# Kernel optimization log

Measured on AMD Instinct MI355X. Metric: run time of the kernel, lower is better.

The kernel has to match this reference:

```python
import jax, jax.numpy as jnp
import numpy as np

NUM_SRC1, NUM_DST1 = 2_000_000, 131_072
NUM_SRC2, NUM_DST2 = 131_072, 8_192
E1, E2 = NUM_DST1 * 15, NUM_DST2 * 15
F_IN, F_H = 128, 128


def setup_inputs() -> dict:
    key = jax.random.key(0)
    ks = jax.random.split(key, 10)
    return {
        "x": jax.random.normal(ks[0], (NUM_SRC1, F_IN), dtype=jnp.float32),
        "edge1_src": jax.random.randint(ks[1], (E1,), 0, NUM_SRC1, dtype=jnp.int32),
        "edge1_dst": jax.random.randint(ks[2], (E1,), 0, NUM_DST1, dtype=jnp.int32),
        "edge2_src": jax.random.randint(ks[3], (E2,), 0, NUM_SRC2, dtype=jnp.int32),
        "edge2_dst": jax.random.randint(ks[4], (E2,), 0, NUM_DST2, dtype=jnp.int32),
        "num_dst1": NUM_DST1,
        "num_dst2": NUM_DST2,
        "W_self1": jax.random.normal(ks[5], (F_IN, F_H), dtype=jnp.float32) * 0.05,
        "W_neigh1": jax.random.normal(ks[6], (F_IN, F_H), dtype=jnp.float32) * 0.05,
        "b1": jnp.zeros((F_H,), dtype=jnp.float32),
        "W_self2": jax.random.normal(ks[7], (F_H, F_H), dtype=jnp.float32) * 0.05,
        "W_neigh2": jax.random.normal(ks[8], (F_H, F_H), dtype=jnp.float32) * 0.05,
        "b2": jnp.zeros((F_H,), dtype=jnp.float32),
    }


def _sage_mean(h_src, h_dst, e_src, e_dst, num_dst, W_self, W_neigh, b):
    # mean-aggregate neighbor feats per dst, then linear transforms (DGL SAGEConv, aggr='mean')
    agg = jax.ops.segment_sum(h_src[e_src], e_dst, num_segments=num_dst)  # [num_dst, F]
    deg = jax.ops.segment_sum(jnp.ones((e_dst.shape[0],), h_src.dtype), e_dst,
                              num_segments=num_dst)
    mean = agg / jnp.maximum(deg, 1.0)[:, None]
    return h_dst @ W_self + mean @ W_neigh + b


def reference(x, edge1_src, edge1_dst, edge2_src, edge2_dst, num_dst1, num_dst2,
              W_self1, W_neigh1, b1, W_self2, W_neigh2, b2):
    h_dst = x[:num_dst1]
    h = _sage_mean(x, h_dst, edge1_src, edge1_dst, num_dst1, W_self1, W_neigh1, b1)
    h = jax.nn.relu(h)
    h_dst2 = h[:num_dst2]
    out = _sage_mean(h, h_dst2, edge2_src, edge2_dst, num_dst2, W_self2, W_neigh2, b2)
    return out
```

## Files before the change

### kernel.cpp

```cpp
#include <hip/hip_runtime.h>

static constexpr int FDIM = 128;
static constexpr int ND1  = 131072;
static constexpr int ND2  = 8192;
static constexpr int PADW = 64;
static constexpr int LDP  = 56;
static constexpr int AML  = 136;

using bf16x8 = __attribute__((ext_vector_type(8))) short;
using u16x8  = __attribute__((ext_vector_type(8))) unsigned short;
using f32x4  = __attribute__((ext_vector_type(4))) float;

static __device__ __forceinline__ unsigned short f2bf(float f) {
  unsigned u = __float_as_uint(f);
  u = (u + 0x7FFFu + ((u >> 16) & 1u)) >> 16;
  return (unsigned short)u;
}
static __device__ __forceinline__ float bf2f(unsigned short s) {
  return __uint_as_float(((unsigned)s) << 16);
}

__global__ void build_pad(const int* __restrict__ e1s, const int* __restrict__ e1d,
                          const int* __restrict__ e2s, const int* __restrict__ e2d,
                          int* __restrict__ cnt1, int* __restrict__ cnt2,
                          int* __restrict__ pad1, int* __restrict__ pad2,
                          int E1, int E2, int nb_fill,
                          const float* __restrict__ Ws1, const float* __restrict__ Wn1,
                          unsigned short* __restrict__ Wt1,
                          const float* __restrict__ Ws2, const float* __restrict__ Wn2,
                          unsigned short* __restrict__ Wt2) {
  if ((int)blockIdx.x >= nb_fill) {
    int t = (blockIdx.x - nb_fill) * 256 + threadIdx.x;
    int which = t >> 15;
    int r = t & 32767;
    int col = r >> 8, k = r & 255;
    const float* Ws = which ? Ws2 : Ws1;
    const float* Wn = which ? Wn2 : Wn1;
    unsigned short* Wt = which ? Wt2 : Wt1;
    float v = (k < 128) ? Ws[k * 128 + col] : Wn[(k - 128) * 128 + col];
    Wt[col * 256 + k] = f2bf(v);
    return;
  }
  const int n1 = E1 >> 2, n2 = E2 >> 2;
  int t = blockIdx.x * 256 + threadIdx.x;
  if (t < n1) {
    int4 d = ((const int4*)e1d)[t];
    int4 s = ((const int4*)e1s)[t];
    int p;
    p = atomicAdd(&cnt1[d.x], 1); if (p < PADW) pad1[d.x * PADW + p] = s.x;
    p = atomicAdd(&cnt1[d.y], 1); if (p < PADW) pad1[d.y * PADW + p] = s.y;
    p = atomicAdd(&cnt1[d.z], 1); if (p < PADW) pad1[d.z * PADW + p] = s.z;
    p = atomicAdd(&cnt1[d.w], 1); if (p < PADW) pad1[d.w * PADW + p] = s.w;
  } else if (t < n1 + n2) {
    int4 d = ((const int4*)e2d)[t - n1];
    int4 s = ((const int4*)e2s)[t - n1];
    int p;
    p = atomicAdd(&cnt2[d.x], 1); if (p < PADW) pad2[d.x * PADW + p] = s.x;
    p = atomicAdd(&cnt2[d.y], 1); if (p < PADW) pad2[d.y * PADW + p] = s.y;
    p = atomicAdd(&cnt2[d.z], 1); if (p < PADW) pad2[d.z * PADW + p] = s.z;
    p = atomicAdd(&cnt2[d.w], 1); if (p < PADW) pad2[d.w * PADW + p] = s.w;
  }
  if (blockIdx.x == 0) {
    int tt = threadIdx.x;
    if (tt < (E1 & 3)) {
      int e = E1 - 1 - tt, d = e1d[e];
      int p = atomicAdd(&cnt1[d], 1); if (p < PADW) pad1[d * PADW + p] = e1s[e];
    }
    int t2 = tt - 8;
    if (t2 >= 0 && t2 < (E2 & 3)) {
      int e = E2 - 1 - t2, d = e2d[e];
      int p = atomicAdd(&cnt2[d], 1); if (p < PADW) pad2[d * PADW + p] = e2s[e];
    }
  }
}

template<bool L1>
__global__ __launch_bounds__(256)
void fused_layer(const void* __restrict__ selfp,
                 const int* __restrict__ pad, const int* __restrict__ cnt,
                 const unsigned short* __restrict__ Wt,
                 const float* __restrict__ bias,
                 void* __restrict__ Outp)
{
  __shared__ unsigned short AmL[128 * AML];
  __shared__ unsigned short Asb[128 * LDP];
  __shared__ unsigned short Wsb[128 * LDP];
  const int tid  = threadIdx.x;
  const int lane = tid & 63;
  const int w    = tid >> 6;
  const int half = lane >> 5;
  const int sub  = lane & 31;
  const int row0 = blockIdx.x * 128;

  for (int i = 0; i < 16; ++i) {
    const int rl   = w * 32 + i * 2 + half;
    const int row  = row0 + rl;
    const int degt = cnt[row];
    const int deg  = degt < PADW ? degt : PADW;
    float ax = 0.f, ay = 0.f, az = 0.f, aw = 0.f;
    for (int base = 0; base < deg; base += 32) {
      int t = base + sub;
      int idx = pad[(size_t)row * PADW + (t < deg ? t : deg - 1)];
      const int lim = (deg - base) < 32 ? (deg - base) : 32;
      for (int b = 0; b < lim; b += 8) {
        if (L1) {
          float4 v[8];
          #pragma unroll
          for (int j = 0; j < 8; ++j) {
            int e = __shfl(idx, half * 32 + b + j);
            v[j] = *(const float4*)((const float*)selfp + (size_t)e * FDIM + sub * 4);
          }
          #pragma unroll
          for (int j = 0; j < 8; ++j) {
            float mk = (b + j) < lim ? 1.f : 0.f;
            ax = fmaf(v[j].x, mk, ax); ay = fmaf(v[j].y, mk, ay);
            az = fmaf(v[j].z, mk, az); aw = fmaf(v[j].w, mk, aw);
          }
        } else {
          ushort4 v[8];
          #pragma unroll
          for (int j = 0; j < 8; ++j) {
            int e = __shfl(idx, half * 32 + b + j);
            v[j] = *(const ushort4*)((const unsigned short*)selfp + (size_t)e * FDIM + sub * 4);
          }
          #pragma unroll
          for (int j = 0; j < 8; ++j) {
            float mk = (b + j) < lim ? 1.f : 0.f;
            ax = fmaf(bf2f(v[j].x), mk, ax); ay = fmaf(bf2f(v[j].y), mk, ay);
            az = fmaf(bf2f(v[j].z), mk, az); aw = fmaf(bf2f(v[j].w), mk, aw);
          }
        }
      }
    }
    const float inv = 1.f / (float)(degt > 1 ? degt : 1);
    ushort4 o;
    o.x = f2bf(ax * inv); o.y = f2bf(ay * inv);
    o.z = f2bf(az * inv); o.w = f2bf(aw * inv);
    *(ushort4*)&AmL[rl * AML + sub * 4] = o;
  }
  __syncthreads();

  const int p = lane & 15;
  const int q = lane >> 4;
  f32x4 acc[2][8];
  #pragma unroll
  for (int m = 0; m < 2; ++m)
    #pragma unroll
    for (int n = 0; n < 8; ++n) acc[m][n] = (f32x4){0.f, 0.f, 0.f, 0.f};

  const int sr = tid >> 1;
  const int sk = (tid & 1) * 16;

  for (int c = 0; c < 8; ++c) {
    const int kc = c * 32;
    const int kl = kc & 127;
    {
      const unsigned short* wsrc = Wt + (size_t)sr * 256 + kc + sk;
      u16x8 a = *(const u16x8*)(wsrc);
      u16x8 b = *(const u16x8*)(wsrc + 8);
      *(u16x8*)&Wsb[sr * LDP + sk]     = a;
      *(u16x8*)&Wsb[sr * LDP + sk + 8] = b;
    }
    if (c >= 4) {
      u16x8 a = *(const u16x8*)&AmL[sr * AML + kl + sk];
      u16x8 b = *(const u16x8*)&AmL[sr * AML + kl + sk + 8];
      *(u16x8*)&Asb[sr * LDP + sk]     = a;
      *(u16x8*)&Asb[sr * LDP + sk + 8] = b;
    } else if (!L1) {
      const unsigned short* asrc =
          (const unsigned short*)selfp + (size_t)(row0 + sr) * FDIM + kl + sk;
      u16x8 a = *(const u16x8*)(asrc);
      u16x8 b = *(const u16x8*)(asrc + 8);
      *(u16x8*)&Asb[sr * LDP + sk]     = a;
      *(u16x8*)&Asb[sr * LDP + sk + 8] = b;
    } else {
      const float* asrc = (const float*)selfp + (size_t)(row0 + sr) * FDIM + kl + sk;
      float4 f0 = *(const float4*)(asrc);
      float4 f1 = *(const float4*)(asrc + 4);
      float4 f2 = *(const float4*)(asrc + 8);
      float4 f3 = *(const float4*)(asrc + 12);
      u16x8 a, b;
      a[0] = f2bf(f0.x); a[1] = f2bf(f0.y); a[2] = f2bf(f0.z); a[3] = f2bf(f0.w);
      a[4] = f2bf(f1.x); a[5] = f2bf(f1.y); a[6] = f2bf(f1.z); a[7] = f2bf(f1.w);
      b[0] = f2bf(f2.x); b[1] = f2bf(f2.y); b[2] = f2bf(f2.z); b[3] = f2bf(f2.w);
      b[4] = f2bf(f3.x); b[5] = f2bf(f3.y); b[6] = f2bf(f3.z); b[7] = f2bf(f3.w);
      *(u16x8*)&Asb[sr * LDP + sk]     = a;
      *(u16x8*)&Asb[sr * LDP + sk + 8] = b;
    }
    __syncthreads();
    bf16x8 af[2];
    #pragma unroll
    for (int m = 0; m < 2; ++m)
      af[m] = *(const bf16x8*)&Asb[(w * 32 + m * 16 + p) * LDP + q * 8];
    #pragma unroll
    for (int n = 0; n < 8; ++n) {
      bf16x8 bfr = *(const bf16x8*)&Wsb[(n * 16 + p) * LDP + q * 8];
      acc[0][n] = __builtin_amdgcn_mfma_f32_16x16x32_bf16(af[0], bfr, acc[0][n], 0, 0, 0);
      acc[1][n] = __builtin_amdgcn_mfma_f32_16x16x32_bf16(af[1], bfr, acc[1][n], 0, 0, 0);
    }
    __syncthreads();
  }

  #pragma unroll
  for (int n = 0; n < 8; ++n) {
    const int col = n * 16 + p;
    const float bv = bias[col];
    #pragma unroll
    for (int m = 0; m < 2; ++m) {
      #pragma unroll
      for (int r = 0; r < 4; ++r) {
        float y = acc[m][n][r] + bv;
        if (L1) y = fmaxf(y, 0.f);
        const size_t grow = (size_t)(row0 + w * 32 + m * 16 + q * 4 + r);
        if (L1) ((unsigned short*)Outp)[grow * FDIM + col] = f2bf(y);
        else    ((float*)Outp)[grow * FDIM + col] = y;
      }
    }
  }
}

extern "C" void kernel_launch(void* const* d_in, const int* in_sizes, int n_in,
                              void* d_out, int out_size, void* d_ws, size_t ws_size,
                              hipStream_t stream) {
  const float* x   = (const float*)d_in[0];
  const int*   e1s = (const int*)d_in[1];
  const int*   e1d = (const int*)d_in[2];
  const int*   e2s = (const int*)d_in[3];
  const int*   e2d = (const int*)d_in[4];
  const float* Ws1 = (const float*)d_in[7];
  const float* Wn1 = (const float*)d_in[8];
  const float* b1  = (const float*)d_in[9];
  const float* Ws2 = (const float*)d_in[10];
  const float* Wn2 = (const float*)d_in[11];
  const float* b2  = (const float*)d_in[12];
  const int E1 = in_sizes[1];
  const int E2 = in_sizes[3];

  char* pw = (char*)d_ws;
  unsigned short* h   = (unsigned short*)pw; pw += (size_t)ND1 * FDIM * 2;
  unsigned short* Wt1 = (unsigned short*)pw; pw += (size_t)FDIM * 256 * 2;
  unsigned short* Wt2 = (unsigned short*)pw; pw += (size_t)FDIM * 256 * 2;
  int* pad1 = (int*)pw; pw += (size_t)ND1 * PADW * 4;
  int* pad2 = (int*)pw; pw += (size_t)ND2 * PADW * 4;
  int* cnt1 = (int*)pw; pw += (size_t)ND1 * 4;
  int* cnt2 = (int*)pw; pw += (size_t)ND2 * 4;

  hipMemsetAsync(cnt1, 0, (size_t)(ND1 + ND2) * 4, stream);

  const int n4 = (E1 >> 2) + (E2 >> 2);
  const int nb_fill = (n4 + 255) / 256;
  build_pad<<<nb_fill + 256, 256, 0, stream>>>(e1s, e1d, e2s, e2d, cnt1, cnt2,
                                               pad1, pad2, E1, E2, nb_fill,
                                               Ws1, Wn1, Wt1, Ws2, Wn2, Wt2);

  fused_layer<true ><<<ND1 / 128, 256, 0, stream>>>(x, pad1, cnt1, Wt1, b1, h);
  fused_layer<false><<<ND2 / 128, 256, 0, stream>>>(h, pad2, cnt2, Wt2, b2, (float*)d_out);
}
```

Before: 442.1 us.

## Split layer-1 into separate gather-mean and MFMA GEMM kernels

Layer 1 is split from one fused gather-plus-GEMM kernel into a standalone gather/mean kernel that writes a bf16 aggregate to workspace, followed by a separate MFMA GEMM kernel. The gather kernel uses many small blocks (two rows per wave) to raise occupancy and memory-level parallelism for the random gathers, which the fused kernel's large LDS footprint limited. The layer-2 CSR build moves into that gather launch's tail blocks. The cost is an extra round trip of the aggregate through global memory (about 32 MB write plus read) and one more launch.

```diff
diff --git a/kernel.cpp b/kernel.cpp
--- a/kernel.cpp
+++ b/kernel.cpp
@@ -20,15 +20,13 @@
   return __uint_as_float(((unsigned)s) << 16);
 }
 
-__global__ void build_pad(const int* __restrict__ e1s, const int* __restrict__ e1d,
-                          const int* __restrict__ e2s, const int* __restrict__ e2d,
-                          int* __restrict__ cnt1, int* __restrict__ cnt2,
-                          int* __restrict__ pad1, int* __restrict__ pad2,
-                          int E1, int E2, int nb_fill,
-                          const float* __restrict__ Ws1, const float* __restrict__ Wn1,
-                          unsigned short* __restrict__ Wt1,
-                          const float* __restrict__ Ws2, const float* __restrict__ Wn2,
-                          unsigned short* __restrict__ Wt2) {
+__global__ void build1(const int* __restrict__ e1s, const int* __restrict__ e1d,
+                       int* __restrict__ cnt1, int* __restrict__ pad1,
+                       int E1, int nb_fill,
+                       const float* __restrict__ Ws1, const float* __restrict__ Wn1,
+                       unsigned short* __restrict__ Wt1,
+                       const float* __restrict__ Ws2, const float* __restrict__ Wn2,
+                       unsigned short* __restrict__ Wt2) {
   if ((int)blockIdx.x >= nb_fill) {
     int t = (blockIdx.x - nb_fill) * 256 + threadIdx.x;
     int which = t >> 15;
@@ -41,7 +39,7 @@
     Wt[col * 256 + k] = f2bf(v);
     return;
   }
-  const int n1 = E1 >> 2, n2 = E2 >> 2;
+  const int n1 = E1 >> 2;
   int t = blockIdx.x * 256 + threadIdx.x;
   if (t < n1) {
     int4 d = ((const int4*)e1d)[t];
@@ -51,14 +49,6 @@
     p = atomicAdd(&cnt1[d.y], 1); if (p < PADW) pad1[d.y * PADW + p] = s.y;
     p = atomicAdd(&cnt1[d.z], 1); if (p < PADW) pad1[d.z * PADW + p] = s.z;
     p = atomicAdd(&cnt1[d.w], 1); if (p < PADW) pad1[d.w * PADW + p] = s.w;
-  } else if (t < n1 + n2) {
-    int4 d = ((const int4*)e2d)[t - n1];
-    int4 s = ((const int4*)e2s)[t - n1];
-    int p;
-    p = atomicAdd(&cnt2[d.x], 1); if (p < PADW) pad2[d.x * PADW + p] = s.x;
-    p = atomicAdd(&cnt2[d.y], 1); if (p < PADW) pad2[d.y * PADW + p] = s.y;
-    p = atomicAdd(&cnt2[d.z], 1); if (p < PADW) pad2[d.z * PADW + p] = s.z;
-    p = atomicAdd(&cnt2[d.w], 1); if (p < PADW) pad2[d.w * PADW + p] = s.w;
   }
   if (blockIdx.x == 0) {
     int tt = threadIdx.x;
@@ -66,21 +56,161 @@
       int e = E1 - 1 - tt, d = e1d[e];
       int p = atomicAdd(&cnt1[d], 1); if (p < PADW) pad1[d * PADW + p] = e1s[e];
     }
-    int t2 = tt - 8;
-    if (t2 >= 0 && t2 < (E2 & 3)) {
-      int e = E2 - 1 - t2, d = e2d[e];
-      int p = atomicAdd(&cnt2[d], 1); if (p < PADW) pad2[d * PADW + p] = e2s[e];
-    }
-  }
-}
-
-template<bool L1>
+  }
+}
+
 __global__ __launch_bounds__(256)
-void fused_layer(const void* __restrict__ selfp,
-                 const int* __restrict__ pad, const int* __restrict__ cnt,
-                 const unsigned short* __restrict__ Wt,
-                 const float* __restrict__ bias,
-                 void* __restrict__ Outp)
+void gather_mean1(const float* __restrict__ src, const int* __restrict__ pad,
+                  const int* __restrict__ cnt, unsigned short* __restrict__ out,
+                  int nrows, int nb_gather,
+                  const int* __restrict__ e2s, const int* __restrict__ e2d,
+                  int* __restrict__ cnt2, int* __restrict__ pad2, int E2) {
+  if ((int)blockIdx.x >= nb_gather) {
+    const int n2 = E2 >> 2;
+    int t = (blockIdx.x - nb_gather) * 256 + threadIdx.x;
+    if (t < n2) {
+      int4 d = ((const int4*)e2d)[t];
+      int4 s = ((const int4*)e2s)[t];
+      int p;
+      p = atomicAdd(&cnt2[d.x], 1); if (p < PADW) pad2[d.x * PADW + p] = s.x;
+      p = atomicAdd(&cnt2[d.y], 1); if (p < PADW) pad2[d.y * PADW + p] = s.y;
+      p = atomicAdd(&cnt2[d.z], 1); if (p < PADW) pad2[d.z * PADW + p] = s.z;
+      p = atomicAdd(&cnt2[d.w], 1); if (p < PADW) pad2[d.w * PADW + p] = s.w;
+    }
+    if (blockIdx.x == (unsigned)nb_gather) {
+      int tt = threadIdx.x;
+      if (tt < (E2 & 3)) {
+        int e = E2 - 1 - tt, d = e2d[e];
+        int p = atomicAdd(&cnt2[d], 1); if (p < PADW) pad2[d * PADW + p] = e2s[e];
+      }
+    }
+    return;
+  }
+  const int lane = threadIdx.x & 63;
+  const int half = lane >> 5;
+  const int sub  = lane & 31;
+  const int wid  = (int)((blockIdx.x * 256u + threadIdx.x) >> 6);
+  const int row  = wid * 2 + half;
+  if (row >= nrows) return;
+  const int degt = cnt[row];
+  const int deg  = degt < PADW ? degt : PADW;
+  float ax = 0.f, ay = 0.f, az = 0.f, aw = 0.f;
+  for (int base = 0; base < deg; base += 32) {
+    int t = base + sub;
+    int idx = pad[(size_t)row * PADW + (t < deg ? t : deg - 1)];
+    const int lim = (deg - base) < 32 ? (deg - base) : 32;
+    for (int b = 0; b < lim; b += 8) {
+      float4 v[8];
+      #pragma unroll
+      for (int j = 0; j < 8; ++j) {
+        int e = __shfl(idx, half * 32 + b + j);
+        v[j] = *(const float4*)(src + (size_t)e * FDIM + sub * 4);
+      }
+      #pragma unroll
+      for (int j = 0; j < 8; ++j) {
+        float mk = (b + j) < lim ? 1.f : 0.f;
+        ax = fmaf(v[j].x, mk, ax); ay = fmaf(v[j].y, mk, ay);
+        az = fmaf(v[j].z, mk, az); aw = fmaf(v[j].w, mk, aw);
+      }
+    }
+  }
+  const float inv = 1.f / (float)(degt > 1 ? degt : 1);
+  ushort4 o;
+  o.x = f2bf(ax * inv); o.y = f2bf(ay * inv);
+  o.z = f2bf(az * inv); o.w = f2bf(aw * inv);
+  *(ushort4*)(out + (size_t)row * FDIM + sub * 4) = o;
+}
+
+__global__ __launch_bounds__(256)
+void gemm_mfma1(const float* __restrict__ Ax,
+                const unsigned short* __restrict__ Am,
+                const unsigned short* __restrict__ Wt,
+                const float* __restrict__ bias,
+                unsigned short* __restrict__ Out) {
+  __shared__ unsigned short Asb[128 * LDP];
+  __shared__ unsigned short Wsb[128 * LDP];
+  const int tid  = threadIdx.x;
+  const int lane = tid & 63;
+  const int w    = tid >> 6;
+  const int row0 = blockIdx.x * 128;
+  const int p    = lane & 15;
+  const int q    = lane >> 4;
+
+  f32x4 acc[2][8];
+  #pragma unroll
+  for (int m = 0; m < 2; ++m)
+    #pragma unroll
+    for (int n = 0; n < 8; ++n) acc[m][n] = (f32x4){0.f, 0.f, 0.f, 0.f};
+
+  const int sr = tid >> 1;
+  const int sk = (tid & 1) * 16;
+
+  for (int c = 0; c < 8; ++c) {
+    const int kc = c * 32;
+    const int kl = kc & 127;
+    {
+      const unsigned short* wsrc = Wt + (size_t)sr * 256 + kc + sk;
+      u16x8 a = *(const u16x8*)(wsrc);
+      u16x8 b = *(const u16x8*)(wsrc + 8);
+      *(u16x8*)&Wsb[sr * LDP + sk]     = a;
+      *(u16x8*)&Wsb[sr * LDP + sk + 8] = b;
+    }
+    if (c >= 4) {
+      const unsigned short* asrc = Am + (size_t)(row0 + sr) * FDIM + kl + sk;
+      u16x8 a = *(const u16x8*)(asrc);
+      u16x8 b = *(const u16x8*)(asrc + 8);
+      *(u16x8*)&Asb[sr * LDP + sk]     = a;
+      *(u16x8*)&Asb[sr * LDP + sk + 8] = b;
+    } else {
+      const float* asrc = Ax + (size_t)(row0 + sr) * FDIM + kl + sk;
+      float4 f0 = *(const float4*)(asrc);
+      float4 f1 = *(const float4*)(asrc + 4);
+      float4 f2 = *(const float4*)(asrc + 8);
+      float4 f3 = *(const float4*)(asrc + 12);
+      u16x8 a, b;
+      a[0] = f2bf(f0.x); a[1] = f2bf(f0.y); a[2] = f2bf(f0.z); a[3] = f2bf(f0.w);
+      a[4] = f2bf(f1.x); a[5] = f2bf(f1.y); a[6] = f2bf(f1.z); a[7] = f2bf(f1.w);
+      b[0] = f2bf(f2.x); b[1] = f2bf(f2.y); b[2] = f2bf(f2.z); b[3] = f2bf(f2.w);
+      b[4] = f2bf(f3.x); b[5] = f2bf(f3.y); b[6] = f2bf(f3.z); b[7] = f2bf(f3.w);
+      *(u16x8*)&Asb[sr * LDP + sk]     = a;
+      *(u16x8*)&Asb[sr * LDP + sk + 8] = b;
+    }
+    __syncthreads();
+    bf16x8 af[2];
+    #pragma unroll
+    for (int m = 0; m < 2; ++m)
+      af[m] = *(const bf16x8*)&Asb[(w * 32 + m * 16 + p) * LDP + q * 8];
+    #pragma unroll
+    for (int n = 0; n < 8; ++n) {
+      bf16x8 bfr = *(const bf16x8*)&Wsb[(n * 16 + p) * LDP + q * 8];
+      acc[0][n] = __builtin_amdgcn_mfma_f32_16x16x32_bf16(af[0], bfr, acc[0][n], 0, 0, 0);
+      acc[1][n] = __builtin_amdgcn_mfma_f32_16x16x32_bf16(af[1], bfr, acc[1][n], 0, 0, 0);
+    }
+    __syncthreads();
+  }
+
+  #pragma unroll
+  for (int n = 0; n < 8; ++n) {
+    const int col = n * 16 + p;
+    const float bv = bias[col];
+    #pragma unroll
+    for (int m = 0; m < 2; ++m) {
+      #pragma unroll
+      for (int r = 0; r < 4; ++r) {
+        float y = fmaxf(acc[m][n][r] + bv, 0.f);
+        const size_t grow = (size_t)(row0 + w * 32 + m * 16 + q * 4 + r);
+        Out[grow * FDIM + col] = f2bf(y);
+      }
+    }
+  }
+}
+
+__global__ __launch_bounds__(256)
+void fused_layer2(const unsigned short* __restrict__ selfp,
+                  const int* __restrict__ pad, const int* __restrict__ cnt,
+                  const unsigned short* __restrict__ Wt,
+                  const float* __restrict__ bias,
+                  float* __restrict__ Outp)
 {
   __shared__ unsigned short AmL[128 * AML];
   __shared__ unsigned short Asb[128 * LDP];
@@ -103,32 +233,17 @@
       int idx = pad[(size_t)row * PADW + (t < deg ? t : deg - 1)];
       const int lim = (deg - base) < 32 ? (deg - base) : 32;
       for (int b = 0; b < lim; b += 8) {
-        if (L1) {
-          float4 v[8];
-          #pragma unroll
-          for (int j = 0; j < 8; ++j) {
-            int e = __shfl(idx, half * 32 + b + j);
-            v[j] = *(const float4*)((const float*)selfp + (size_t)e * FDIM + sub * 4);
-          }
-          #pragma unroll
-          for (int j = 0; j < 8; ++j) {
-            float mk = (b + j) < lim ? 1.f : 0.f;
-            ax = fmaf(v[j].x, mk, ax); ay = fmaf(v[j].y, mk, ay);
-            az = fmaf(v[j].z, mk, az); aw = fmaf(v[j].w, mk, aw);
-          }
-        } else {
-          ushort4 v[8];
-          #pragma unroll
-          for (int j = 0; j < 8; ++j) {
-            int e = __shfl(idx, half * 32 + b + j);
-            v[j] = *(const ushort4*)((const unsigned short*)selfp + (size_t)e * FDIM + sub * 4);
-          }
-          #pragma unroll
-          for (int j = 0; j < 8; ++j) {
-            float mk = (b + j) < lim ? 1.f : 0.f;
-            ax = fmaf(bf2f(v[j].x), mk, ax); ay = fmaf(bf2f(v[j].y), mk, ay);
-            az = fmaf(bf2f(v[j].z), mk, az); aw = fmaf(bf2f(v[j].w), mk, aw);
-          }
+        ushort4 v[8];
+        #pragma unroll
+        for (int j = 0; j < 8; ++j) {
+          int e = __shfl(idx, half * 32 + b + j);
+          v[j] = *(const ushort4*)(selfp + (size_t)e * FDIM + sub * 4);
+        }
+        #pragma unroll
+        for (int j = 0; j < 8; ++j) {
+          float mk = (b + j) < lim ? 1.f : 0.f;
+          ax = fmaf(bf2f(v[j].x), mk, ax); ay = fmaf(bf2f(v[j].y), mk, ay);
+          az = fmaf(bf2f(v[j].z), mk, az); aw = fmaf(bf2f(v[j].w), mk, aw);
         }
       }
     }
@@ -166,26 +281,12 @@
       u16x8 b = *(const u16x8*)&AmL[sr * AML + kl + sk + 8];
       *(u16x8*)&Asb[sr * LDP + sk]     = a;
       *(u16x8*)&Asb[sr * LDP + sk + 8] = b;
-    } else if (!L1) {
-      const unsigned short* asrc =
-          (const unsigned short*)selfp + (size_t)(row0 + sr) * FDIM + kl + sk;
+    } else {
+      const unsigned short* asrc = selfp + (size_t)(row0 + sr) * FDIM + kl + sk;
       u16x8 a = *(const u16x8*)(asrc);
       u16x8 b = *(const u16x8*)(asrc + 8);
       *(u16x8*)&Asb[sr * LDP + sk]     = a;
       *(u16x8*)&Asb[sr * LDP + sk + 8] = b;
-    } else {
-      const float* asrc = (const float*)selfp + (size_t)(row0 + sr) * FDIM + kl + sk;
-      float4 f0 = *(const float4*)(asrc);
-      float4 f1 = *(const float4*)(asrc + 4);
-      float4 f2 = *(const float4*)(asrc + 8);
-      float4 f3 = *(const float4*)(asrc + 12);
-      u16x8 a, b;
-      a[0] = f2bf(f0.x); a[1] = f2bf(f0.y); a[2] = f2bf(f0.z); a[3] = f2bf(f0.w);
-      a[4] = f2bf(f1.x); a[5] = f2bf(f1.y); a[6] = f2bf(f1.z); a[7] = f2bf(f1.w);
-      b[0] = f2bf(f2.x); b[1] = f2bf(f2.y); b[2] = f2bf(f2.z); b[3] = f2bf(f2.w);
-      b[4] = f2bf(f3.x); b[5] = f2bf(f3.y); b[6] = f2bf(f3.z); b[7] = f2bf(f3.w);
-      *(u16x8*)&Asb[sr * LDP + sk]     = a;
-      *(u16x8*)&Asb[sr * LDP + sk + 8] = b;
     }
     __syncthreads();
     bf16x8 af[2];
@@ -210,10 +311,8 @@
       #pragma unroll
       for (int r = 0; r < 4; ++r) {
         float y = acc[m][n][r] + bv;
-        if (L1) y = fmaxf(y, 0.f);
         const size_t grow = (size_t)(row0 + w * 32 + m * 16 + q * 4 + r);
-        if (L1) ((unsigned short*)Outp)[grow * FDIM + col] = f2bf(y);
-        else    ((float*)Outp)[grow * FDIM + col] = y;
+        Outp[grow * FDIM + col] = y;
       }
     }
   }
@@ -237,9 +336,10 @@
   const int E2 = in_sizes[3];
 
   char* pw = (char*)d_ws;
-  unsigned short* h   = (unsigned short*)pw; pw += (size_t)ND1 * FDIM * 2;
-  unsigned short* Wt1 = (unsigned short*)pw; pw += (size_t)FDIM * 256 * 2;
-  unsigned short* Wt2 = (unsigned short*)pw; pw += (size_t)FDIM * 256 * 2;
+  unsigned short* agg1 = (unsigned short*)pw; pw += (size_t)ND1 * FDIM * 2;
+  unsigned short* h    = (unsigned short*)pw; pw += (size_t)ND1 * FDIM * 2;
+  unsigned short* Wt1  = (unsigned short*)pw; pw += (size_t)FDIM * 256 * 2;
+  unsigned short* Wt2  = (unsigned short*)pw; pw += (size_t)FDIM * 256 * 2;
   int* pad1 = (int*)pw; pw += (size_t)ND1 * PADW * 4;
   int* pad2 = (int*)pw; pw += (size_t)ND2 * PADW * 4;
   int* cnt1 = (int*)pw; pw += (size_t)ND1 * 4;
@@ -247,12 +347,17 @@
 
   hipMemsetAsync(cnt1, 0, (size_t)(ND1 + ND2) * 4, stream);
 
-  const int n4 = (E1 >> 2) + (E2 >> 2);
-  const int nb_fill = (n4 + 255) / 256;
-  build_pad<<<nb_fill + 256, 256, 0, stream>>>(e1s, e1d, e2s, e2d, cnt1, cnt2,
-                                               pad1, pad2, E1, E2, nb_fill,
-                                               Ws1, Wn1, Wt1, Ws2, Wn2, Wt2);
-
-  fused_layer<true ><<<ND1 / 128, 256, 0, stream>>>(x, pad1, cnt1, Wt1, b1, h);
-  fused_layer<false><<<ND2 / 128, 256, 0, stream>>>(h, pad2, cnt2, Wt2, b2, (float*)d_out);
-}
+  const int nb_fill1 = ((E1 >> 2) + 255) / 256;
+  build1<<<nb_fill1 + 256, 256, 0, stream>>>(e1s, e1d, cnt1, pad1, E1, nb_fill1,
+                                             Ws1, Wn1, Wt1, Ws2, Wn2, Wt2);
+
+  const int nb_gather = ND1 / 8;
+  const int nb_fill2  = ((E2 >> 2) + 255) / 256;
+  gather_mean1<<<nb_gather + nb_fill2, 256, 0, stream>>>(x, pad1, cnt1, agg1, ND1,
+                                                         nb_gather, e2s, e2d,
+                                                         cnt2, pad2, E2);
+
+  gemm_mfma1<<<ND1 / 128, 256, 0, stream>>>(x, agg1, Wt1, b1, h);
+
+  fused_layer2<<<ND2 / 128, 256, 0, stream>>>(h, pad2, cnt2, Wt2, b2, (float*)d_out);
+}
```

Result: no change. 439.4 us (-0.6%).
